# Kernel optimization log

Measured on AMD Instinct MI355X. Metric: run time of the kernel, lower is better.

## Reference

```python
import jax, jax.numpy as jnp
import numpy as np

AREA = 4
NUM_HEADS = 4


def _conv1x1(x, w, s, t):
    # 1x1 Conv (bias=False) + folded BatchNorm: per-out-channel scale s, shift t
    y = jnp.einsum('bchw,oc->bohw', x, w)
    return y * s[None, :, None, None] + t[None, :, None, None]


def setup_inputs() -> dict:
    key = jax.random.key(0)
    ks = jax.random.split(key, 9)
    C, heads = 128, NUM_HEADS
    x = jax.random.normal(ks[0], (2, C, 80, 80), jnp.float32)

    def wmat(k, o, i):
        return jax.random.normal(k, (o, i), jnp.float32) * (i ** -0.5)

    def bn(k, n):
        k1, k2 = jax.random.split(k)
        s = 1.0 + 0.05 * jax.random.normal(k1, (n,), jnp.float32)
        t = 0.05 * jax.random.normal(k2, (n,), jnp.float32)
        return s, t

    w_qk = wmat(ks[1], 2 * C, C); s_qk, t_qk = bn(ks[2], 2 * C)
    w_in = wmat(ks[3], C, C); s_in, t_in = bn(ks[4], C)
    w_out = wmat(ks[5], C, C); s_out, t_out = bn(ks[6], C)
    w_fg = jax.random.normal(ks[7], (heads, heads, 1, 5), jnp.float32) * ((5 * heads) ** -0.5)
    s_fg, t_fg = bn(ks[8], heads)
    return dict(x=x, w_qk=w_qk, s_qk=s_qk, t_qk=t_qk, w_in=w_in, s_in=s_in,
                t_in=t_in, w_out=w_out, s_out=s_out, t_out=t_out,
                w_fg=w_fg, s_fg=s_fg, t_fg=t_fg)


def reference(x, w_qk, s_qk, t_qk, w_in, s_in, t_in, w_out, s_out, t_out, w_fg, s_fg, t_fg):
    B, C, H, W = x.shape
    N = H * W
    heads = NUM_HEADS
    hd = C // heads
    inp = x
    # qk projection -> [B, N, 2C]
    qk = _conv1x1(x, w_qk, s_qk, t_qk).reshape(B, 2 * C, N).transpose(0, 2, 1)
    # input-gated values -> [B, N, C]
    v = jax.nn.sigmoid(_conv1x1(x, w_in, s_in, t_in)) * x
    v = v.reshape(B, C, N).transpose(0, 2, 1)
    # area split
    Be, Na = B * AREA, N // AREA
    qk = qk.reshape(Be, Na, 2 * C)
    v = v.reshape(Be, Na, C)
    q, k = qk[..., :C], qk[..., C:]
    q = q.transpose(0, 2, 1).reshape(Be, heads, hd, Na)
    k = k.transpose(0, 2, 1).reshape(Be, heads, hd, Na)
    v = v.transpose(0, 2, 1).reshape(Be, heads, hd, Na)
    # full NxN attention per area/head
    attn = jnp.einsum('bhdn,bhdm->bhnm', q, k) * (hd ** -0.5)
    attn = jax.nn.softmax(attn, axis=-1)
    # forget gate: (1,5) conv mixing heads along last axis, pad (0,2), BN fold, SiLU
    attn = jax.lax.conv_general_dilated(attn, w_fg, (1, 1), ((0, 0), (2, 2)),
                                        dimension_numbers=('NCHW', 'OIHW', 'NCHW'))
    attn = attn * s_fg[None, :, None, None] + t_fg[None, :, None, None]
    attn = jax.nn.silu(attn)
    # v @ attn^T -> [Be, heads, hd, Na]
    o = jnp.einsum('bhdj,bhij->bhdi', v, attn)
    # merge areas back: [Be,Na,h,hd] -> [B,N,C] -> [B,C,H,W]
    o = o.transpose(0, 3, 1, 2).reshape(B, N, C)
    o = o.reshape(B, H, W, C).transpose(0, 3, 1, 2)
    return jax.nn.sigmoid(_conv1x1(o, w_out, s_out, t_out)) * o + inp
```

## Files before the change

### kernel.cpp

```cpp
#include <hip/hip_runtime.h>
#include <hip/hip_bf16.h>
#include <cstdint>

#define CC 128
#define NN 6400
#define NAa 1600
#define HEADS 4
#define HD 32
#define NB 32
#define MT 64

#define P_ROW 68
#define P_HEAD 1096
#define A_ROW 76
#define A_HEAD 1224
#define PW (HEADS * P_HEAD)
#define AW (HEADS * A_HEAD)

typedef __attribute__((ext_vector_type(8))) short bfrag8;
typedef __attribute__((ext_vector_type(4))) float ffrag4;
typedef union { uint2 u2[2]; bfrag8 f8; } cvt16;

#define LOG2E 1.4426950408889634f
#define QSCL (0.17677669529663687f * 1.4426950408889634f)

__device__ __forceinline__ float sigmoid_fast(float y) {
  return __builtin_amdgcn_rcpf(1.0f + __builtin_amdgcn_exp2f(-LOG2E * y));
}
__device__ __forceinline__ unsigned short f2bf(float f) {
  unsigned u = __float_as_uint(f);
  return (unsigned short)((u + 0x7FFFu + ((u >> 16) & 1u)) >> 16);
}
__device__ __forceinline__ unsigned pack_bf16(float a, float b) {
  return (unsigned)f2bf(a) | ((unsigned)f2bf(b) << 16);
}
__device__ __forceinline__ unsigned pk2(float a, float b) {
  float2 f2; f2.x = a; f2.y = b;
  __hip_bfloat162 h = __float22bfloat162_rn(f2);
  union { __hip_bfloat162 h2; unsigned u; } cv; cv.h2 = h;
  return cv.u;
}
__device__ __forceinline__ float bfl(unsigned u) { return __uint_as_float(u << 16); }
__device__ __forceinline__ float bfh(unsigned u) { return __uint_as_float(u & 0xFFFF0000u); }

__global__ __launch_bounds__(256) void prep_kernel(
    const float* __restrict__ x, const float* __restrict__ w_qk,
    const float* __restrict__ s_qk, const float* __restrict__ w_in,
    const float* __restrict__ s_in, const float* __restrict__ w_out,
    const float* __restrict__ s_out,
    unsigned short* __restrict__ xt, unsigned short* __restrict__ wqkb,
    unsigned short* __restrict__ wob) {
  __shared__ float tile[32][33];
  const int blk = blockIdx.x, tid = threadIdx.x;
  if (blk < 1600) {
    const int b = blk / 800, rem = blk - b * 800;
    const int ct = rem / 200, pt2 = rem - ct * 200;
    const int c0 = ct * 32, px0 = pt2 * 32;
    for (int i = tid; i < 1024; i += 256) {
      int r = i >> 5, p = i & 31;
      tile[r][p] = x[((size_t)(b * CC + c0 + r)) * NN + px0 + p];
    }
    __syncthreads();
    for (int i = tid; i < 512; i += 256) {
      int px = i >> 4, cp = i & 15;
      unsigned pk = pk2(tile[2 * cp][px], tile[2 * cp + 1][px]);
      *(unsigned*)&xt[((size_t)b * NN + px0 + px) * CC + c0 + 2 * cp] = pk;
    }
  } else if (blk < 1608) {
    const int r0 = (blk - 1600) * 48;
    for (int i = tid; i < 6144; i += 256) {
      int r = r0 + (i >> 7), c = i & 127;
      float wv, sv;
      if (r < 2 * CC) { wv = w_qk[r * CC + c]; sv = s_qk[r] * (r < CC ? QSCL : 1.0f); }
      else           { wv = w_in[(r - 2 * CC) * CC + c]; sv = s_in[r - 2 * CC]; }
      wqkb[r * CC + c] = f2bf(wv * sv);
    }
  } else {
    const int r0 = (blk - 1608) * 64;
    for (int i = tid; i < 8192; i += 256) {
      int r = r0 + (i >> 7), c = i & 127;
      wob[r * CC + c] = f2bf(w_out[r * CC + c] * s_out[r]);
    }
  }
}

__global__ __launch_bounds__(256) void qkv_kernel(
    const unsigned short* __restrict__ xt, const unsigned short* __restrict__ wqkb,
    const float* __restrict__ t_qk, const float* __restrict__ t_in,
    unsigned short* __restrict__ qt, unsigned short* __restrict__ kt,
    unsigned short* __restrict__ vb) {
  const int tid = threadIdx.x;
  const int w = tid >> 6, lane = tid & 63, lo = lane & 15, g = lane >> 4;
  const int blk = blockIdx.x;
  const int b = blk / 400, pt = blk - b * 400;
  const int ng0 = pt * 16;
  const int a = ng0 / NAa, na0 = ng0 - a * NAa;
  const int be = b * 4 + a;
  const size_t xrow = ((size_t)b * NN + ng0 + lo) * CC;
  bfrag8 bf[4];
#pragma unroll
  for (int kk = 0; kk < 4; kk++) bf[kk] = *(const bfrag8*)&xt[xrow + kk * 32 + g * 8];
#pragma unroll
  for (int mt6 = 0; mt6 < 6; mt6++) {
    const int rowbase = (w * 6 + mt6) * 16;
    ffrag4 d = {0.f, 0.f, 0.f, 0.f};
#pragma unroll
    for (int kk = 0; kk < 4; kk++) {
      bfrag8 af = *(const bfrag8*)&wqkb[(size_t)(rowbase + lo) * CC + kk * 32 + g * 8];
      d = __builtin_amdgcn_mfma_f32_16x16x32_bf16(af, bf[kk], d, 0, 0, 0);
    }
    const int r0c = rowbase + 4 * g;
    if (r0c < CC) {
      const int h = r0c >> 5, d0 = r0c & 31;
      uint2 pk;
      pk.x = pk2(d[0] + t_qk[r0c] * QSCL, d[1] + t_qk[r0c + 1] * QSCL);
      pk.y = pk2(d[2] + t_qk[r0c + 2] * QSCL, d[3] + t_qk[r0c + 3] * QSCL);
      *(uint2*)&qt[((size_t)(be * HEADS + h) * NAa + na0 + lo) * HD + d0] = pk;
    } else if (r0c < 2 * CC) {
      const int ch = r0c - CC, h = ch >> 5, d0 = ch & 31;
      uint2 pk;
      pk.x = pk2(d[0] + t_qk[r0c], d[1] + t_qk[r0c + 1]);
      pk.y = pk2(d[2] + t_qk[r0c + 2], d[3] + t_qk[r0c + 3]);
      *(uint2*)&kt[((size_t)(be * HEADS + h) * NAa + na0 + lo) * HD + d0] = pk;
    } else {
      const int ch0 = r0c - 2 * CC;
      const uint2 xv = *(const uint2*)&xt[xrow + ch0];
      float xr[4] = {bfl(xv.x), bfh(xv.x), bfl(xv.y), bfh(xv.y)};
#pragma unroll
      for (int r = 0; r < 4; r++) {
        float y = d[r] + t_in[ch0 + r];
        vb[((size_t)be * CC + ch0 + r) * NAa + na0 + lo] = f2bf(sigmoid_fast(y) * xr[r]);
      }
    }
  }
}

__global__ __launch_bounds__(256) void stats_kernel(
    const unsigned short* __restrict__ qt, const unsigned short* __restrict__ kt,
    float* __restrict__ pstats) {
  int tid = threadIdx.x;
  int h = tid >> 6, lane = tid & 63, lo = lane & 15, g = lane >> 4;
  int bid = blockIdx.x;
  int be = bid & 7;
  int rest = bid >> 3;
  int n0 = (rest % 100) * 16;
  int split = rest / 100;
  int ts0 = split ? 12 : 0, ts1 = split ? 25 : 12;

  const unsigned short* qtb = qt + (size_t)(be * HEADS + h) * NAa * HD;
  const unsigned short* ktb = kt + (size_t)(be * HEADS + h) * NAa * HD;

  bfrag8 qf = *(const bfrag8*)(qtb + (size_t)(n0 + lo) * HD + g * 8);
  float sm[4] = {0.f, 0.f, 0.f, 0.f};
  for (int t = ts0; t < ts1; t++) {
    int m0 = t * MT;
#pragma unroll
    for (int sb = 0; sb < 4; sb++) {
      bfrag8 kf = *(const bfrag8*)(ktb + (size_t)(m0 + sb * 16 + lo) * HD + g * 8);
      ffrag4 z = {0.f, 0.f, 0.f, 0.f};
      ffrag4 c = __builtin_amdgcn_mfma_f32_16x16x32_bf16(qf, kf, z, 0, 0, 0);
#pragma unroll
      for (int r = 0; r < 4; r++) sm[r] += __builtin_amdgcn_exp2f(c[r]);
    }
  }
#pragma unroll
  for (int r = 0; r < 4; r++) {
#pragma unroll
    for (int off = 1; off <= 8; off <<= 1) sm[r] += __shfl_xor(sm[r], off);
  }
  if (lo == 0) {
    float4 s4; s4.x = sm[0]; s4.y = sm[1]; s4.z = sm[2]; s4.w = sm[3];
    *(float4*)&pstats[((size_t)(split * 8 + be) * HEADS + h) * NAa + n0 + 4 * g] = s4;
  }
}

__global__ __launch_bounds__(512) void apply_kernel(
    const unsigned short* __restrict__ qt, const unsigned short* __restrict__ kt,
    const unsigned short* __restrict__ vb, const float* __restrict__ pstats,
    const float* __restrict__ w_fg, const float* __restrict__ s_fg,
    const float* __restrict__ t_fg, unsigned short* __restrict__ o_part) {
  __shared__ __align__(16) unsigned short Pb[2][2 * PW];
  __shared__ __align__(16) unsigned short A2s[2 * AW];
  const int tid = threadIdx.x;
  const int w = tid >> 6, lane = tid & 63, lo = lane & 15, g = lane >> 4;
  const int h = w >> 1, u = w & 1;
  const int bid = blockIdx.x;
  const int be = bid & 7;
  const int rest = bid >> 3;
  const int n0 = (rest % 50) * NB;
  const int split = rest / 50;
  const int ts0 = split ? 12 : 0;
  const int tend = split ? 26 : 12;

  const unsigned short* qtb = qt + (size_t)(be * HEADS + h) * NAa * HD;
  const unsigned short* ktb = kt + (size_t)(be * HEADS + h) * NAa * HD;
  const unsigned short* vhb = vb + (size_t)(be * CC + h * HD) * NAa;

  bfrag8 qf[2];
#pragma unroll
  for (int qs = 0; qs < 2; ++qs)
    qf[qs] = *(const bfrag8*)(qtb + (size_t)(n0 + 16 * qs + lo) * HD + g * 8);

  bfrag8 wfrag;
  {
    const int ho = lo >> 2, s = lo & 3;
#pragma unroll
    for (int j = 0; j < 8; j++) {
      const int tp = j - s;
      float wv = (tp >= 0 && tp < 5) ? w_fg[(ho * HEADS + g) * 5 + tp] : 0.0f;
      wfrag[j] = (short)f2bf(wv);
    }
  }
  const float sfv = s_fg[g], tfv = t_fg[g];

  float inv[2];
#pragma unroll
  for (int qs = 0; qs < 2; ++qs)
    inv[qs] = 1.0f / (pstats[((size_t)(0 + be) * HEADS + h) * NAa + n0 + 16 * qs + lo] +
                      pstats[((size_t)(8 + be) * HEADS + h) * NAa + n0 + 16 * qs + lo]);

  ffrag4 oacc[2][2];
#pragma unroll
  for (int qs = 0; qs < 2; ++qs) {
    ffrag4 z = {0.f, 0.f, 0.f, 0.f};
    oacc[qs][0] = z; oacc[qs][1] = z;
  }

  unsigned short* P0 = Pb[0];
  if (split == 0) {
    if (u == 0 && g == 0) {
      uint2 zz; zz.x = 0; zz.y = 0;
#pragma unroll
      for (int qs = 0; qs < 2; ++qs)
        *(uint2*)&P0[qs * PW + h * P_HEAD + lo * P_ROW] = zz;
    }
  } else if (u == 0) {
    bfrag8 kf = *(const bfrag8*)(ktb + (size_t)(752 + lo) * HD + g * 8);
#pragma unroll
    for (int qs = 0; qs < 2; ++qs) {
      ffrag4 z = {0.f, 0.f, 0.f, 0.f};
      ffrag4 c = __builtin_amdgcn_mfma_f32_16x16x32_bf16(kf, qf[qs], z, 0, 0, 0);
      if (g == 3) {
        uint2 pk;
        pk.x = pk2(__builtin_amdgcn_exp2f(c[0]) * inv[qs], __builtin_amdgcn_exp2f(c[1]) * inv[qs]);
        pk.y = pk2(__builtin_amdgcn_exp2f(c[2]) * inv[qs], __builtin_amdgcn_exp2f(c[3]) * inv[qs]);
        *(uint2*)&P0[qs * PW + h * P_HEAD + lo * P_ROW] = pk;
      }
    }
  }
  {
    const int m0 = ts0 * MT;
#pragma unroll
    for (int sbi = 0; sbi < 2; sbi++) {
      const int sb = 2 * u + sbi;
      bfrag8 kf = *(const bfrag8*)(ktb + (size_t)(m0 + sb * 16 + lo) * HD + g * 8);
#pragma unroll
      for (int qs = 0; qs < 2; ++qs) {
        ffrag4 z = {0.f, 0.f, 0.f, 0.f};
        ffrag4 c = __builtin_amdgcn_mfma_f32_16x16x32_bf16(kf, qf[qs], z, 0, 0, 0);
        uint2 pk;
        pk.x = pk2(__builtin_amdgcn_exp2f(c[0]) * inv[qs], __builtin_amdgcn_exp2f(c[1]) * inv[qs]);
        pk.y = pk2(__builtin_amdgcn_exp2f(c[2]) * inv[qs], __builtin_amdgcn_exp2f(c[3]) * inv[qs]);
        *(uint2*)&P0[qs * PW + h * P_HEAD + lo * P_ROW + 16 * sb + 4 * g + 4] = pk;
      }
    }
  }
  __syncthreads();

  int cur = 0;
  for (int t = ts0; t < tend; t++) {
    const int m0 = t * MT;
    const bfrag8 vf0 = *(const bfrag8*)(vhb + (size_t)lo * NAa + (m0 - 2 + 32 * u + 8 * g));
    const bfrag8 vf1 = *(const bfrag8*)(vhb + (size_t)(16 + lo) * NAa + (m0 - 2 + 32 * u + 8 * g));
    const bool doqk = (t + 1 < tend);
    const bool realqk = doqk && (t + 1 < 25);
    bfrag8 kf0, kf1;
    if (realqk) {
      const int m1 = (t + 1) * MT;
      kf0 = *(const bfrag8*)(ktb + (size_t)(m1 + (2 * u) * 16 + lo) * HD + g * 8);
      kf1 = *(const bfrag8*)(ktb + (size_t)(m1 + (2 * u + 1) * 16 + lo) * HD + g * 8);
    }
    unsigned short* Pc = Pb[cur];
    unsigned short* Pn = Pb[cur ^ 1];
    if (doqk) {
#pragma unroll
      for (int qs = 0; qs < 2; ++qs) {
        uint2 hh = *(const uint2*)&Pc[qs * PW + g * P_HEAD + lo * P_ROW + 64];
        *(uint2*)&Pn[qs * PW + g * P_HEAD + lo * P_ROW] = hh;
      }
      if (realqk) {
#pragma unroll
        for (int qs = 0; qs < 2; ++qs) {
          ffrag4 z = {0.f, 0.f, 0.f, 0.f};
          ffrag4 c0 = __builtin_amdgcn_mfma_f32_16x16x32_bf16(kf0, qf[qs], z, 0, 0, 0);
          ffrag4 c1 = __builtin_amdgcn_mfma_f32_16x16x32_bf16(kf1, qf[qs], z, 0, 0, 0);
          uint2 pk;
          pk.x = pk2(__builtin_amdgcn_exp2f(c0[0]) * inv[qs], __builtin_amdgcn_exp2f(c0[1]) * inv[qs]);
          pk.y = pk2(__builtin_amdgcn_exp2f(c0[2]) * inv[qs], __builtin_amdgcn_exp2f(c0[3]) * inv[qs]);
          *(uint2*)&Pn[qs * PW + h * P_HEAD + lo * P_ROW + 16 * (2 * u) + 4 * g + 4] = pk;
          pk.x = pk2(__builtin_amdgcn_exp2f(c1[0]) * inv[qs], __builtin_amdgcn_exp2f(c1[1]) * inv[qs]);
          pk.y = pk2(__builtin_amdgcn_exp2f(c1[2]) * inv[qs], __builtin_amdgcn_exp2f(c1[3]) * inv[qs]);
          *(uint2*)&Pn[qs * PW + h * P_HEAD + lo * P_ROW + 16 * (2 * u + 1) + 4 * g + 4] = pk;
        }
      } else {
        uint2 zz; zz.x = 0; zz.y = 0;
#pragma unroll
        for (int qs = 0; qs < 2; ++qs) {
          *(uint2*)&Pn[qs * PW + h * P_HEAD + lo * P_ROW + 16 * (2 * u) + 4 * g + 4] = zz;
          *(uint2*)&Pn[qs * PW + h * P_HEAD + lo * P_ROW + 16 * (2 * u + 1) + 4 * g + 4] = zz;
        }
      }
    }
    const bool edge = (t == 0) || (t == 25);
#pragma unroll
    for (int qs = 0; qs < 2; ++qs) {
#pragma unroll
      for (int ii = 0; ii < 2; ii++) {
        const int i = 2 * w + ii;
        cvt16 bb;
        bb.u2[0] = *(const uint2*)&Pc[qs * PW + g * P_HEAD + lo * P_ROW + 4 * i];
        bb.u2[1] = *(const uint2*)&Pc[qs * PW + g * P_HEAD + lo * P_ROW + 4 * i + 4];
        ffrag4 z = {0.f, 0.f, 0.f, 0.f};
        ffrag4 d = __builtin_amdgcn_mfma_f32_16x16x32_bf16(wfrag, bb.f8, z, 0, 0, 0);
        float a2v[4];
        if (edge) {
#pragma unroll
          for (int r = 0; r < 4; r++) {
            const int mp = m0 - 2 + 4 * i + r;
            float y = d[r] * sfv + tfv;
            float v = y * sigmoid_fast(y);
            a2v[r] = (mp >= 0 && mp < NAa) ? v : 0.0f;
          }
        } else {
#pragma unroll
          for (int r = 0; r < 4; r++) {
            float y = d[r] * sfv + tfv;
            a2v[r] = y * sigmoid_fast(y);
          }
        }
        uint2 pk;
        pk.x = pk2(a2v[0], a2v[1]);
        pk.y = pk2(a2v[2], a2v[3]);
        *(uint2*)&A2s[qs * AW + g * A_HEAD + lo * A_ROW + 4 * i] = pk;
      }
    }
    __syncthreads();
#pragma unroll
    for (int qs = 0; qs < 2; ++qs) {
      cvt16 av;
      av.u2[0] = *(const uint2*)&A2s[qs * AW + h * A_HEAD + lo * A_ROW + 32 * u + 8 * g];
      av.u2[1] = *(const uint2*)&A2s[qs * AW + h * A_HEAD + lo * A_ROW + 32 * u + 8 * g + 4];
      oacc[qs][0] = __builtin_amdgcn_mfma_f32_16x16x32_bf16(av.f8, vf0, oacc[qs][0], 0, 0, 0);
      oacc[qs][1] = __builtin_amdgcn_mfma_f32_16x16x32_bf16(av.f8, vf1, oacc[qs][1], 0, 0, 0);
    }
    __syncthreads();
    cur ^= 1;
  }

  float* scr = (float*)A2s;
  if (u == 1) {
#pragma unroll
    for (int qs = 0; qs < 2; ++qs) {
      float4 f0; f0.x = oacc[qs][0][0]; f0.y = oacc[qs][0][1]; f0.z = oacc[qs][0][2]; f0.w = oacc[qs][0][3];
      float4 f1; f1.x = oacc[qs][1][0]; f1.y = oacc[qs][1][1]; f1.z = oacc[qs][1][2]; f1.w = oacc[qs][1][3];
      *(float4*)&scr[((qs * 4 + h) * 64 + lane) * 8] = f0;
      *(float4*)&scr[((qs * 4 + h) * 64 + lane) * 8 + 4] = f1;
    }
  }
  __syncthreads();
  if (u == 0) {
#pragma unroll
    for (int qs = 0; qs < 2; ++qs) {
      const float4 f0 = *(const float4*)&scr[((qs * 4 + h) * 64 + lane) * 8];
      const float4 f1 = *(const float4*)&scr[((qs * 4 + h) * 64 + lane) * 8 + 4];
      const float fa[4] = {f0.x, f0.y, f0.z, f0.w};
      const float fb[4] = {f1.x, f1.y, f1.z, f1.w};
#pragma unroll
      for (int r = 0; r < 4; r++) {
        const size_t rowoff = ((size_t)(split * 8 + be) * NAa + n0 + 16 * qs + 4 * g + r) * CC;
        o_part[rowoff + h * HD + lo] = f2bf(oacc[qs][0][r] + fa[r]);
        o_part[rowoff + h * HD + 16 + lo] = f2bf(oacc[qs][1][r] + fb[r]);
      }
    }
  }
}

__global__ __launch_bounds__(256) void out_kernel(
    const unsigned short* __restrict__ o_part, const unsigned short* __restrict__ wob,
    const float* __restrict__ t_out, const float* __restrict__ x,
    float* __restrict__ out) {
  const int tid = threadIdx.x;
  const int w = tid >> 6, lane = tid & 63, lo = lane & 15, g = lane >> 4;
  const int blk = blockIdx.x;
  const int b = blk / 400, pt = blk - b * 400;
  const int ng0 = pt * 16;
  const int a = ng0 / NAa, na0 = ng0 - a * NAa;
  const int be = b * 4 + a;
  const size_t orow0 = ((size_t)(0 * 8 + be) * NAa + na0 + lo) * CC;
  const size_t orow1 = ((size_t)(1 * 8 + be) * NAa + na0 + lo) * CC;
  bfrag8 bf0[4], bf1[4];
#pragma unroll
  for (int kk = 0; kk < 4; kk++) {
    bf0[kk] = *(const bfrag8*)&o_part[orow0 + kk * 32 + g * 8];
    bf1[kk] = *(const bfrag8*)&o_part[orow1 + kk * 32 + g * 8];
  }
#pragma unroll
  for (int mt2 = 0; mt2 < 2; mt2++) {
    const int rowbase = (w * 2 + mt2) * 16;
    ffrag4 d = {0.f, 0.f, 0.f, 0.f};
#pragma unroll
    for (int kk = 0; kk < 4; kk++) {
      bfrag8 af = *(const bfrag8*)&wob[(size_t)(rowbase + lo) * CC + kk * 32 + g * 8];
      d = __builtin_amdgcn_mfma_f32_16x16x32_bf16(af, bf0[kk], d, 0, 0, 0);
      d = __builtin_amdgcn_mfma_f32_16x16x32_bf16(af, bf1[kk], d, 0, 0, 0);
    }
    const int ch0 = rowbase + 4 * g;
    const uint2 q0 = *(const uint2*)&o_part[orow0 + ch0];
    const uint2 q1 = *(const uint2*)&o_part[orow1 + ch0];
    float ov[4] = {bfl(q0.x) + bfl(q1.x), bfh(q0.x) + bfh(q1.x),
                   bfl(q0.y) + bfl(q1.y), bfh(q0.y) + bfh(q1.y)};
#pragma unroll
    for (int r = 0; r < 4; r++) {
      const size_t xi = ((size_t)b * CC + ch0 + r) * NN + ng0 + lo;
      float y = d[r] + t_out[ch0 + r];
      out[xi] = ov[r] * sigmoid_fast(y) + x[xi];
    }
  }
}

extern "C" void kernel_launch(void* const* d_in, const int* in_sizes, int n_in,
                              void* d_out, int out_size, void* d_ws, size_t ws_size,
                              hipStream_t stream) {
  const float* x    = (const float*)d_in[0];
  const float* w_qk = (const float*)d_in[1];
  const float* s_qk = (const float*)d_in[2];
  const float* t_qk = (const float*)d_in[3];
  const float* w_in = (const float*)d_in[4];
  const float* s_in = (const float*)d_in[5];
  const float* t_in = (const float*)d_in[6];
  const float* w_out = (const float*)d_in[7];
  const float* s_out = (const float*)d_in[8];
  const float* t_out = (const float*)d_in[9];
  const float* w_fg = (const float*)d_in[10];
  const float* s_fg = (const float*)d_in[11];
  const float* t_fg = (const float*)d_in[12];

  char* wsb = (char*)d_ws;
  unsigned short* o_part = (unsigned short*)wsb;
  unsigned short* vb_raw = (unsigned short*)(wsb + 6553600);
  unsigned short* vbp = vb_raw + 2;
  unsigned short* qt = (unsigned short*)(wsb + 9830464);
  unsigned short* kt = (unsigned short*)(wsb + 13107264);
  unsigned short* xt = (unsigned short*)(wsb + 16384064);
  unsigned short* wqkb = (unsigned short*)(wsb + 19660864);
  unsigned short* wob = (unsigned short*)(wsb + 19759168);
  float* pstats = (float*)(wsb + 19791936);
  float* out = (float*)d_out;

  prep_kernel<<<1610, 256, 0, stream>>>(x, w_qk, s_qk, w_in, s_in, w_out, s_out, xt, wqkb, wob);
  qkv_kernel<<<800, 256, 0, stream>>>(xt, wqkb, t_qk, t_in, qt, kt, vbp);
  stats_kernel<<<1600, 256, 0, stream>>>(qt, kt, pstats);
  apply_kernel<<<800, 512, 0, stream>>>(qt, kt, vbp, pstats, w_fg, s_fg, t_fg, o_part);
  out_kernel<<<800, 256, 0, stream>>>(o_part, wob, t_out, x, out);
}
```

Before: 142.0 us.

## Single-buffer P tile with small halo buffer and reorder QK into gate phase

Replaces the double-buffered probability tile with a single buffer plus a small parity-indexed halo buffer holding the 4-column overlap. The next tile's QK/exp work now runs between the two barriers, so it overlaps the PV MFMAs instead of preceding the conv stage. The halo copy between buffers is removed. Shared memory use drops, and launch bounds now request 8 blocks per CU to raise occupancy, at the risk of register spilling under the tighter register budget.

```diff
diff --git a/kernel.cpp b/kernel.cpp
--- a/kernel.cpp
+++ b/kernel.cpp
@@ -16,6 +16,7 @@
 #define A_HEAD 1224
 #define PW (HEADS * P_HEAD)
 #define AW (HEADS * A_HEAD)
+#define HB_IDX(par, qs, hh, lo) (((((par)*2 + (qs))*4 + (hh))*16 + (lo)) * 4)
 
 typedef __attribute__((ext_vector_type(8))) short bfrag8;
 typedef __attribute__((ext_vector_type(4))) float ffrag4;
@@ -174,13 +175,14 @@
   }
 }
 
-__global__ __launch_bounds__(512) void apply_kernel(
+__global__ __launch_bounds__(512, 8) void apply_kernel(
     const unsigned short* __restrict__ qt, const unsigned short* __restrict__ kt,
     const unsigned short* __restrict__ vb, const float* __restrict__ pstats,
     const float* __restrict__ w_fg, const float* __restrict__ s_fg,
     const float* __restrict__ t_fg, unsigned short* __restrict__ o_part) {
-  __shared__ __align__(16) unsigned short Pb[2][2 * PW];
+  __shared__ __align__(16) unsigned short Ps[2 * PW];
   __shared__ __align__(16) unsigned short A2s[2 * AW];
+  __shared__ __align__(16) unsigned short Hb[1024];
   const int tid = threadIdx.x;
   const int w = tid >> 6, lane = tid & 63, lo = lane & 15, g = lane >> 4;
   const int h = w >> 1, u = w & 1;
@@ -226,13 +228,12 @@
     oacc[qs][0] = z; oacc[qs][1] = z;
   }
 
-  unsigned short* P0 = Pb[0];
   if (split == 0) {
     if (u == 0 && g == 0) {
       uint2 zz; zz.x = 0; zz.y = 0;
 #pragma unroll
       for (int qs = 0; qs < 2; ++qs)
-        *(uint2*)&P0[qs * PW + h * P_HEAD + lo * P_ROW] = zz;
+        *(uint2*)&Hb[HB_IDX(0, qs, h, lo)] = zz;
     }
   } else if (u == 0) {
     bfrag8 kf = *(const bfrag8*)(ktb + (size_t)(752 + lo) * HD + g * 8);
@@ -244,7 +245,7 @@
         uint2 pk;
         pk.x = pk2(__builtin_amdgcn_exp2f(c[0]) * inv[qs], __builtin_amdgcn_exp2f(c[1]) * inv[qs]);
         pk.y = pk2(__builtin_amdgcn_exp2f(c[2]) * inv[qs], __builtin_amdgcn_exp2f(c[3]) * inv[qs]);
-        *(uint2*)&P0[qs * PW + h * P_HEAD + lo * P_ROW] = pk;
+        *(uint2*)&Hb[HB_IDX(0, qs, h, lo)] = pk;
       }
     }
   }
@@ -261,15 +262,17 @@
         uint2 pk;
         pk.x = pk2(__builtin_amdgcn_exp2f(c[0]) * inv[qs], __builtin_amdgcn_exp2f(c[1]) * inv[qs]);
         pk.y = pk2(__builtin_amdgcn_exp2f(c[2]) * inv[qs], __builtin_amdgcn_exp2f(c[3]) * inv[qs]);
-        *(uint2*)&P0[qs * PW + h * P_HEAD + lo * P_ROW + 16 * sb + 4 * g + 4] = pk;
+        *(uint2*)&Ps[qs * PW + h * P_HEAD + lo * P_ROW + 16 * sb + 4 * g] = pk;
+        if (sb == 3 && g == 3)
+          *(uint2*)&Hb[HB_IDX(1, qs, h, lo)] = pk;
       }
     }
   }
   __syncthreads();
 
-  int cur = 0;
   for (int t = ts0; t < tend; t++) {
     const int m0 = t * MT;
+    const int par = t & 1;
     const bfrag8 vf0 = *(const bfrag8*)(vhb + (size_t)lo * NAa + (m0 - 2 + 32 * u + 8 * g));
     const bfrag8 vf1 = *(const bfrag8*)(vhb + (size_t)(16 + lo) * NAa + (m0 - 2 + 32 * u + 8 * g));
     const bool doqk = (t + 1 < tend);
@@ -280,37 +283,6 @@
       kf0 = *(const bfrag8*)(ktb + (size_t)(m1 + (2 * u) * 16 + lo) * HD + g * 8);
       kf1 = *(const bfrag8*)(ktb + (size_t)(m1 + (2 * u + 1) * 16 + lo) * HD + g * 8);
     }
-    unsigned short* Pc = Pb[cur];
-    unsigned short* Pn = Pb[cur ^ 1];
-    if (doqk) {
-#pragma unroll
-      for (int qs = 0; qs < 2; ++qs) {
-        uint2 hh = *(const uint2*)&Pc[qs * PW + g * P_HEAD + lo * P_ROW + 64];
-        *(uint2*)&Pn[qs * PW + g * P_HEAD + lo * P_ROW] = hh;
-      }
-      if (realqk) {
-#pragma unroll
-        for (int qs = 0; qs < 2; ++qs) {
-          ffrag4 z = {0.f, 0.f, 0.f, 0.f};
-          ffrag4 c0 = __builtin_amdgcn_mfma_f32_16x16x32_bf16(kf0, qf[qs], z, 0, 0, 0);
-          ffrag4 c1 = __builtin_amdgcn_mfma_f32_16x16x32_bf16(kf1, qf[qs], z, 0, 0, 0);
-          uint2 pk;
-          pk.x = pk2(__builtin_amdgcn_exp2f(c0[0]) * inv[qs], __builtin_amdgcn_exp2f(c0[1]) * inv[qs]);
-          pk.y = pk2(__builtin_amdgcn_exp2f(c0[2]) * inv[qs], __builtin_amdgcn_exp2f(c0[3]) * inv[qs]);
-          *(uint2*)&Pn[qs * PW + h * P_HEAD + lo * P_ROW + 16 * (2 * u) + 4 * g + 4] = pk;
-          pk.x = pk2(__builtin_amdgcn_exp2f(c1[0]) * inv[qs], __builtin_amdgcn_exp2f(c1[1]) * inv[qs]);
-          pk.y = pk2(__builtin_amdgcn_exp2f(c1[2]) * inv[qs], __builtin_amdgcn_exp2f(c1[3]) * inv[qs]);
-          *(uint2*)&Pn[qs * PW + h * P_HEAD + lo * P_ROW + 16 * (2 * u + 1) + 4 * g + 4] = pk;
-        }
-      } else {
-        uint2 zz; zz.x = 0; zz.y = 0;
-#pragma unroll
-        for (int qs = 0; qs < 2; ++qs) {
-          *(uint2*)&Pn[qs * PW + h * P_HEAD + lo * P_ROW + 16 * (2 * u) + 4 * g + 4] = zz;
-          *(uint2*)&Pn[qs * PW + h * P_HEAD + lo * P_ROW + 16 * (2 * u + 1) + 4 * g + 4] = zz;
-        }
-      }
-    }
     const bool edge = (t == 0) || (t == 25);
 #pragma unroll
     for (int qs = 0; qs < 2; ++qs) {
@@ -318,8 +290,11 @@
       for (int ii = 0; ii < 2; ii++) {
         const int i = 2 * w + ii;
         cvt16 bb;
-        bb.u2[0] = *(const uint2*)&Pc[qs * PW + g * P_HEAD + lo * P_ROW + 4 * i];
-        bb.u2[1] = *(const uint2*)&Pc[qs * PW + g * P_HEAD + lo * P_ROW + 4 * i + 4];
+        if (i == 0)
+          bb.u2[0] = *(const uint2*)&Hb[HB_IDX(par, qs, g, lo)];
+        else
+          bb.u2[0] = *(const uint2*)&Ps[qs * PW + g * P_HEAD + lo * P_ROW + 4 * i - 4];
+        bb.u2[1] = *(const uint2*)&Ps[qs * PW + g * P_HEAD + lo * P_ROW + 4 * i];
         ffrag4 z = {0.f, 0.f, 0.f, 0.f};
         ffrag4 d = __builtin_amdgcn_mfma_f32_16x16x32_bf16(wfrag, bb.f8, z, 0, 0, 0);
         float a2v[4];
@@ -345,6 +320,33 @@
       }
     }
     __syncthreads();
+    if (doqk) {
+      if (realqk) {
+#pragma unroll
+        for (int qs = 0; qs < 2; ++qs) {
+          ffrag4 z = {0.f, 0.f, 0.f, 0.f};
+          ffrag4 c0 = __builtin_amdgcn_mfma_f32_16x16x32_bf16(kf0, qf[qs], z, 0, 0, 0);
+          ffrag4 c1 = __builtin_amdgcn_mfma_f32_16x16x32_bf16(kf1, qf[qs], z, 0, 0, 0);
+          uint2 pk;
+          pk.x = pk2(__builtin_amdgcn_exp2f(c0[0]) * inv[qs], __builtin_amdgcn_exp2f(c0[1]) * inv[qs]);
+          pk.y = pk2(__builtin_amdgcn_exp2f(c0[2]) * inv[qs], __builtin_amdgcn_exp2f(c0[3]) * inv[qs]);
+          *(uint2*)&Ps[qs * PW + h * P_HEAD + lo * P_ROW + 16 * (2 * u) + 4 * g] = pk;
+          uint2 pk1;
+          pk1.x = pk2(__builtin_amdgcn_exp2f(c1[0]) * inv[qs], __builtin_amdgcn_exp2f(c1[1]) * inv[qs]);
+          pk1.y = pk2(__builtin_amdgcn_exp2f(c1[2]) * inv[qs], __builtin_amdgcn_exp2f(c1[3]) * inv[qs]);
+          *(uint2*)&Ps[qs * PW + h * P_HEAD + lo * P_ROW + 16 * (2 * u + 1) + 4 * g] = pk1;
+          if (u == 1 && g == 3)
+            *(uint2*)&Hb[HB_IDX(par, qs, h, lo)] = pk1;
+        }
+      } else {
+        uint2 zz; zz.x = 0; zz.y = 0;
+#pragma unroll
+        for (int qs = 0; qs < 2; ++qs) {
+          *(uint2*)&Ps[qs * PW + h * P_HEAD + lo * P_ROW + 16 * (2 * u) + 4 * g] = zz;
+          *(uint2*)&Ps[qs * PW + h * P_HEAD + lo * P_ROW + 16 * (2 * u + 1) + 4 * g] = zz;
+        }
+      }
+    }
 #pragma unroll
     for (int qs = 0; qs < 2; ++qs) {
       cvt16 av;
@@ -354,7 +356,6 @@
       oacc[qs][1] = __builtin_amdgcn_mfma_f32_16x16x32_bf16(av.f8, vf1, oacc[qs][1], 0, 0, 0);
     }
     __syncthreads();
-    cur ^= 1;
   }
 
   float* scr = (float*)A2s;
```

Result: slower. 233.1 us (+64.1%).
